# Performance work log

Measured on AMD Instinct MI355X. Metric: run time of the kernel, lower is better.

The kernel has to match this reference:

```python
import jax, jax.numpy as jnp
import numpy as np

H = 16
D_MODEL = 1024
D_K = D_MODEL // H


def setup_inputs() -> dict:
    key = jax.random.key(0)
    ks = jax.random.split(key, 12)
    B, S = 4, 2048
    scale = 1.0 / np.sqrt(D_MODEL)
    inp = {
        "query": jax.random.normal(ks[0], (B, S, D_MODEL), dtype=jnp.float32),
        "key": jax.random.normal(ks[1], (B, S, D_MODEL), dtype=jnp.float32),
        "value": jax.random.normal(ks[2], (B, S, D_MODEL), dtype=jnp.float32),
        "Wq": jax.random.normal(ks[3], (D_MODEL, D_MODEL), dtype=jnp.float32) * scale,
        "bq": jnp.zeros((D_MODEL,), dtype=jnp.float32),
        "Wk": jax.random.normal(ks[4], (D_MODEL, D_MODEL), dtype=jnp.float32) * scale,
        "bk": jnp.zeros((D_MODEL,), dtype=jnp.float32),
        "Wv": jax.random.normal(ks[5], (D_MODEL, D_MODEL), dtype=jnp.float32) * scale,
        "bv": jnp.zeros((D_MODEL,), dtype=jnp.float32),
        "Wo": jax.random.normal(ks[6], (D_MODEL, D_MODEL), dtype=jnp.float32) * scale,
        "bo": jnp.zeros((D_MODEL,), dtype=jnp.float32),
    }
    return inp


def reference(query, key, value, Wq, bq, Wk, bk, Wv, bv, Wo, bo):
    B, S, _ = query.shape
    # Linear projections (torch Linear: x @ W^T + b), then split heads -> [B,H,S,d_k]
    def proj(x, W, b):
        y = x @ W.T + b
        return y.reshape(B, S, H, D_K).transpose(0, 2, 1, 3)

    q = proj(query, Wq, bq)
    k = proj(key, Wk, bk)
    v = proj(value, Wv, bv)

    # Explicit QK^T / sqrt(d_k), softmax, AV (no mask; dropout = identity in eval)
    scores = jnp.einsum("bhqd,bhkd->bhqk", q, k) / jnp.sqrt(jnp.float32(D_K))
    attn = jax.nn.softmax(scores, axis=-1)
    x = jnp.einsum("bhqk,bhkd->bhqd", attn, v)

    # Merge heads and final output projection
    x = x.transpose(0, 2, 1, 3).reshape(B, S, H * D_K)
    return x @ Wo.T + bo
```

## Files before the change

kernel.cpp:

```cpp
#include <hip/hip_runtime.h>
#include <hip/hip_bf16.h>
#include <stdint.h>

#define BATCH 4
#define SEQ   2048
#define DM    1024
#define NH    16
#define DK    64
#define MROWS (BATCH * SEQ)

#define C1 0.1803368801111204f

typedef __attribute__((ext_vector_type(8))) short short8;
typedef __attribute__((ext_vector_type(4))) float f32x4;
typedef __attribute__((ext_vector_type(4))) float floatv4;
typedef __attribute__((ext_vector_type(4))) unsigned short us4;
typedef __attribute__((ext_vector_type(4))) unsigned int uint4v;

static __device__ __forceinline__ unsigned short f2bf(float f) {
    union { float f; uint32_t u; } c; c.f = f;
    uint32_t u = c.u;
    return (unsigned short)((u + 0x7fffu + ((u >> 16) & 1u)) >> 16);
}

static __device__ __forceinline__ unsigned int cvt_pk_bf16(float a, float b) {
    __hip_bfloat162 h = __float22bfloat162_rn(float2{a, b});
    unsigned int u; __builtin_memcpy(&u, &h, 4); return u;
}

#define AS1C(p) ((const __attribute__((address_space(1))) unsigned int*)(uintptr_t)(const void*)(p))
#define AS3(p)  ((__attribute__((address_space(3))) unsigned int*)(uintptr_t)(void*)(p))

__global__ __launch_bounds__(256) void cvt3_k(const float* __restrict__ a, const float* __restrict__ b,
                                              const float* __restrict__ c,
                                              unsigned short* __restrict__ oa, unsigned short* __restrict__ ob,
                                              unsigned short* __restrict__ oc) {
    const int z = blockIdx.y;
    const float* s = (z == 0) ? a : (z == 1) ? b : c;
    unsigned short* o = (z == 0) ? oa : (z == 1) ? ob : oc;
    int i = blockIdx.x * 256 + threadIdx.x;
    floatv4 v = ((const floatv4*)s)[i];
    us4 w; w.x = f2bf(v.x); w.y = f2bf(v.y); w.z = f2bf(v.z); w.w = f2bf(v.w);
    ((us4*)o)[i] = w;
}

__global__ __launch_bounds__(256) void cvt4_k(const float* __restrict__ a, const float* __restrict__ b,
                                              const float* __restrict__ c, const float* __restrict__ d,
                                              unsigned short* __restrict__ oa, unsigned short* __restrict__ ob,
                                              unsigned short* __restrict__ oc, unsigned short* __restrict__ od) {
    const int z = blockIdx.y;
    const float* s = (z == 0) ? a : (z == 1) ? b : (z == 2) ? c : d;
    unsigned short* o = (z == 0) ? oa : (z == 1) ? ob : (z == 2) ? oc : od;
    int i = blockIdx.x * 256 + threadIdx.x;
    floatv4 v = ((const floatv4*)s)[i];
    us4 w; w.x = f2bf(v.x); w.y = f2bf(v.y); w.z = f2bf(v.z); w.w = f2bf(v.w);
    ((us4*)o)[i] = w;
}

template <int MODE>
static __device__ __forceinline__ void gemm_body(const unsigned short* __restrict__ A,
                                                 const unsigned short* __restrict__ Bw,
                                                 const float* __restrict__ bias,
                                                 void* __restrict__ out, int m0, int n0,
                                                 float scale) {
    const int tid = threadIdx.x;
    const int wave = tid >> 6, lane = tid & 63, quad = lane >> 4, l16 = lane & 15;
    const int wr = wave & 1, wc = wave >> 1;

    __shared__ alignas(16) unsigned short As[128 * 32];
    __shared__ alignas(16) unsigned short Bs[128 * 32];

    f32x4 acc[4][4];
    #pragma unroll
    for (int i = 0; i < 4; i++)
        #pragma unroll
        for (int j = 0; j < 4; j++) acc[i][j] = (f32x4){0.f, 0.f, 0.f, 0.f};

    const int srow = lane >> 2;
    const int scol = (lane & 3) * 8;

    for (int k0 = 0; k0 < DM; k0 += 32) {
        __syncthreads();
        #pragma unroll
        for (int t = 0; t < 2; t++) {
            const int rr = wave * 32 + t * 16;
            __builtin_amdgcn_global_load_lds(AS1C(A  + (size_t)(m0 + rr + srow) * DM + k0 + scol),
                                             AS3(&As[rr * 32]), 16, 0, 0);
            __builtin_amdgcn_global_load_lds(AS1C(Bw + (size_t)(n0 + rr + srow) * DM + k0 + scol),
                                             AS3(&Bs[rr * 32]), 16, 0, 0);
        }
        __syncthreads();

        short8 af[4], bf[4];
        #pragma unroll
        for (int i = 0; i < 4; i++) af[i] = *(const short8*)&As[(wr * 64 + i * 16 + l16) * 32 + quad * 8];
        #pragma unroll
        for (int i = 0; i < 4; i++) bf[i] = *(const short8*)&Bs[(wc * 64 + i * 16 + l16) * 32 + quad * 8];
        #pragma unroll
        for (int i = 0; i < 4; i++)
            #pragma unroll
            for (int j = 0; j < 4; j++)
                acc[i][j] = __builtin_amdgcn_mfma_f32_16x16x32_bf16(af[i], bf[j], acc[i][j], 0, 0, 0);
    }

    #pragma unroll
    for (int j = 0; j < 4; j++) {
        const int n = n0 + wc * 64 + j * 16 + l16;
        const float bv = bias[n];
        #pragma unroll
        for (int i = 0; i < 4; i++) {
            #pragma unroll
            for (int r = 0; r < 4; r++) {
                const int mrow = m0 + wr * 64 + i * 16 + quad * 4 + r;
                float val = (acc[i][j][r] + bv) * scale;
                if (MODE == 0) {
                    int bb = mrow >> 11, ss = mrow & (SEQ - 1), hh = n >> 6, dd = n & (DK - 1);
                    ((unsigned short*)out)[((((size_t)bb * NH + hh) * SEQ + ss) << 6) + dd] = f2bf(val);
                } else {
                    ((float*)out)[(size_t)mrow * DM + n] = val;
                }
            }
        }
    }
}

__global__ __launch_bounds__(256, 2) void gemm_qkv_k(const unsigned short* qa, const unsigned short* ka,
                                                     const unsigned short* va, const unsigned short* wq,
                                                     const unsigned short* wk, const unsigned short* wv,
                                                     const float* bq, const float* bk, const float* bv,
                                                     unsigned short* qh, unsigned short* kh, unsigned short* vh) {
    const int z = blockIdx.z;
    const unsigned short* A = (z == 0) ? qa : (z == 1) ? ka : va;
    const unsigned short* W = (z == 0) ? wq : (z == 1) ? wk : wv;
    const float* bi = (z == 0) ? bq : (z == 1) ? bk : bv;
    unsigned short* o = (z == 0) ? qh : (z == 1) ? kh : vh;
    const float sc = (z == 0) ? C1 : 1.0f;
    gemm_body<0>(A, W, bi, o, blockIdx.x * 128, blockIdx.y * 128, sc);
}

__global__ __launch_bounds__(256, 2) void gemm_o_k(const unsigned short* xb, const unsigned short* wo,
                                                   const float* bo, float* out) {
    gemm_body<1>(xb, wo, bo, out, blockIdx.x * 128, blockIdx.y * 128, 1.0f);
}

__global__ __launch_bounds__(256) void vtrans_k(const unsigned short* __restrict__ Vh,
                                                unsigned short* __restrict__ Vt) {
    const int bh = blockIdx.y;
    const int t0 = blockIdx.x * 128;
    const unsigned short* src = Vh + (size_t)bh * SEQ * DK;
    unsigned short* dst = Vt + (size_t)bh * DK * SEQ;
    #pragma unroll
    for (int it = 0; it < 2; it++) {
        const int id = it * 256 + threadIdx.x;
        const int C8 = id & 15;
        const int dp = id >> 4;
        unsigned int v[8];
        #pragma unroll
        for (int j = 0; j < 8; j++) {
            const int key = ((C8 >> 2) << 5) + ((j >> 2) << 4) + ((C8 & 3) << 2) + (j & 3);
            v[j] = *(const unsigned int*)(src + (size_t)(t0 + key) * DK + dp * 2);
        }
        short8 r0, r1;
        #pragma unroll
        for (int j = 0; j < 8; j++) { r0[j] = (short)(v[j] & 0xffff); r1[j] = (short)(v[j] >> 16); }
        *(short8*)(dst + (size_t)(dp * 2    ) * SEQ + t0 + C8 * 8) = r0;
        *(short8*)(dst + (size_t)(dp * 2 + 1) * SEQ + t0 + C8 * 8) = r1;
    }
}

__global__ __launch_bounds__(256, 4) void flash_attn_k(const unsigned short* __restrict__ Qh,
                                                       const unsigned short* __restrict__ Kh,
                                                       const unsigned short* __restrict__ Vtc,
                                                       unsigned short* __restrict__ Xb) {
    const int tid = threadIdx.x;
    const int wave = tid >> 6, lane = tid & 63, quad = lane >> 4, l16 = lane & 15;
    const int h = blockIdx.y, b = blockIdx.z;
    const unsigned short* Qp = Qh  + (size_t)(b * NH + h) * SEQ * DK;
    const unsigned short* Kp = Kh  + (size_t)(b * NH + h) * SEQ * DK;
    const unsigned short* Vp = Vtc + (size_t)(b * NH + h) * DK * SEQ;
    const int q0 = blockIdx.x * 128 + wave * 32;

    __shared__ alignas(16) unsigned short kt[128][72];
    __shared__ alignas(16) unsigned short vt[64][136];

    short8 aq[2][2];
    #pragma unroll
    for (int m = 0; m < 2; m++)
        #pragma unroll
        for (int kk = 0; kk < 2; kk++)
            aq[m][kk] = *(const short8*)(Qp + (size_t)(q0 + m * 16 + l16) * DK + kk * 32 + quad * 8);

    short8 ones;
    #pragma unroll
    for (int j = 0; j < 8; j++) ones[j] = (short)0x3F80;

    f32x4 O[2][4];
    f32x4 lacc[2];
    #pragma unroll
    for (int m = 0; m < 2; m++) {
        #pragma unroll
        for (int db = 0; db < 4; db++) O[m][db] = (f32x4){0.f, 0.f, 0.f, 0.f};
        lacc[m] = (f32x4){0.f, 0.f, 0.f, 0.f};
    }

    for (int t0 = 0; t0 < SEQ; t0 += 128) {
        __syncthreads();
        #pragma unroll
        for (int it = 0; it < 4; it++) {
            const int id = it * 256 + tid;
            const int key = id >> 3, dg = (id & 7) * 8;
            *(short8*)&kt[key][dg] = *(const short8*)(Kp + (size_t)(t0 + key) * DK + dg);
        }
        #pragma unroll
        for (int it = 0; it < 4; it++) {
            const int id = it * 256 + tid;
            const int d = id >> 4, pc = (id & 15) * 8;
            *(short8*)&vt[d][pc] = *(const short8*)(Vp + (size_t)d * SEQ + t0 + pc);
        }
        __syncthreads();

        #pragma unroll
        for (int t = 0; t < 4; t++) {
            f32x4 s[2][2];
            #pragma unroll
            for (int m = 0; m < 2; m++)
                #pragma unroll
                for (int sb = 0; sb < 2; sb++) s[m][sb] = (f32x4){0.f, 0.f, 0.f, 0.f};

            #pragma unroll
            for (int kk = 0; kk < 2; kk++) {
                short8 bk0 = *(const short8*)&kt[(t * 2    ) * 16 + l16][kk * 32 + quad * 8];
                short8 bk1 = *(const short8*)&kt[(t * 2 + 1) * 16 + l16][kk * 32 + quad * 8];
                s[0][0] = __builtin_amdgcn_mfma_f32_16x16x32_bf16(bk0, aq[0][kk], s[0][0], 0, 0, 0);
                s[0][1] = __builtin_amdgcn_mfma_f32_16x16x32_bf16(bk1, aq[0][kk], s[0][1], 0, 0, 0);
                s[1][0] = __builtin_amdgcn_mfma_f32_16x16x32_bf16(bk0, aq[1][kk], s[1][0], 0, 0, 0);
                s[1][1] = __builtin_amdgcn_mfma_f32_16x16x32_bf16(bk1, aq[1][kk], s[1][1], 0, 0, 0);
            }

            short8 pa[2];
            #pragma unroll
            for (int m = 0; m < 2; m++) {
                uint4v pk;
                pk.x = cvt_pk_bf16(exp2f(s[m][0][0]), exp2f(s[m][0][1]));
                pk.y = cvt_pk_bf16(exp2f(s[m][0][2]), exp2f(s[m][0][3]));
                pk.z = cvt_pk_bf16(exp2f(s[m][1][0]), exp2f(s[m][1][1]));
                pk.w = cvt_pk_bf16(exp2f(s[m][1][2]), exp2f(s[m][1][3]));
                __builtin_memcpy(&pa[m], &pk, 16);
            }

            #pragma unroll
            for (int db = 0; db < 4; db++) {
                short8 vf = *(const short8*)&vt[db * 16 + l16][t * 32 + quad * 8];
                O[0][db] = __builtin_amdgcn_mfma_f32_16x16x32_bf16(pa[0], vf, O[0][db], 0, 0, 0);
                O[1][db] = __builtin_amdgcn_mfma_f32_16x16x32_bf16(pa[1], vf, O[1][db], 0, 0, 0);
            }
            lacc[0] = __builtin_amdgcn_mfma_f32_16x16x32_bf16(pa[0], ones, lacc[0], 0, 0, 0);
            lacc[1] = __builtin_amdgcn_mfma_f32_16x16x32_bf16(pa[1], ones, lacc[1], 0, 0, 0);
        }
    }

    #pragma unroll
    for (int m = 0; m < 2; m++) {
        #pragma unroll
        for (int r = 0; r < 4; r++) {
            const float inv = 1.f / lacc[m][r];
            const int srow = q0 + m * 16 + quad * 4 + r;
            unsigned short* op = Xb + ((size_t)b * SEQ + srow) * DM + h * DK;
            #pragma unroll
            for (int db = 0; db < 4; db++)
                op[db * 16 + l16] = f2bf(O[m][db][r] * inv);
        }
    }
}

extern "C" void kernel_launch(void* const* d_in, const int* in_sizes, int n_in,
                              void* d_out, int out_size, void* d_ws, size_t ws_size,
                              hipStream_t stream) {
    const float* q_in = (const float*)d_in[0];
    const float* k_in = (const float*)d_in[1];
    const float* v_in = (const float*)d_in[2];
    const float* Wq   = (const float*)d_in[3];
    const float* bq   = (const float*)d_in[4];
    const float* Wk   = (const float*)d_in[5];
    const float* bk   = (const float*)d_in[6];
    const float* Wv   = (const float*)d_in[7];
    const float* bv   = (const float*)d_in[8];
    const float* Wo   = (const float*)d_in[9];
    const float* bo   = (const float*)d_in[10];

    const size_t MB = 1024ull * 1024ull;
    char* ws = (char*)d_ws;
    unsigned short* qa  = (unsigned short*)(ws +   0 * MB);
    unsigned short* ka  = (unsigned short*)(ws +  16 * MB);
    unsigned short* va  = (unsigned short*)(ws +  32 * MB);
    unsigned short* wqb = (unsigned short*)(ws +  48 * MB);
    unsigned short* wkb = (unsigned short*)(ws +  50 * MB);
    unsigned short* wvb = (unsigned short*)(ws +  52 * MB);
    unsigned short* wob = (unsigned short*)(ws +  54 * MB);
    unsigned short* qh  = (unsigned short*)(ws +  56 * MB);
    unsigned short* kh  = (unsigned short*)(ws +  72 * MB);
    unsigned short* vh  = (unsigned short*)(ws +  88 * MB);
    unsigned short* xb  = (unsigned short*)(ws + 104 * MB);
    unsigned short* vtc = va;

    cvt3_k<<<dim3(8192, 3), 256, 0, stream>>>(q_in, k_in, v_in, qa, ka, va);
    cvt4_k<<<dim3(1024, 4), 256, 0, stream>>>(Wq, Wk, Wv, Wo, wqb, wkb, wvb, wob);

    gemm_qkv_k<<<dim3(MROWS / 128, DM / 128, 3), 256, 0, stream>>>(qa, ka, va, wqb, wkb, wvb,
                                                                   bq, bk, bv, qh, kh, vh);
    vtrans_k<<<dim3(SEQ / 128, BATCH * NH), 256, 0, stream>>>(vh, vtc);

    flash_attn_k<<<dim3(SEQ / 128, NH, BATCH), 256, 0, stream>>>(qh, kh, vtc, xb);

    gemm_o_k<<<dim3(MROWS / 128, DM / 128), 256, 0, stream>>>(xb, wob, bo, (float*)d_out);
}
```

Before: 387.0 us.

## Fuse V transpose into QKV GEMM epilogue and prefetch K/V tiles in attention

The V projection GEMM now writes its output directly in the transposed, permuted key order the attention kernel expects, so the separate transpose kernel and its extra read and write pass are gone. The flash attention loop now register-prefetches the next K and V tile while the current one is being computed, and it replaces the second __syncthreads with an LDS wait plus a raw barrier. exp2f is swapped for the hardware exp2 builtin. Risks include the key-permutation mapping in the epilogue and a small rise in register pressure from the prefetch buffers.

After: 338.3 us. -12.6%, faster.

```diff
diff --git a/kernel.cpp b/kernel.cpp
--- a/kernel.cpp
+++ b/kernel.cpp
@@ -27,6 +27,8 @@
     __hip_bfloat162 h = __float22bfloat162_rn(float2{a, b});
     unsigned int u; __builtin_memcpy(&u, &h, 4); return u;
 }
+
+static __device__ __forceinline__ float ex2(float x) { return __builtin_amdgcn_exp2f(x); }
 
 #define AS1C(p) ((const __attribute__((address_space(1))) unsigned int*)(uintptr_t)(const void*)(p))
 #define AS3(p)  ((__attribute__((address_space(3))) unsigned int*)(uintptr_t)(void*)(p))
@@ -109,15 +111,26 @@
         const float bv = bias[n];
         #pragma unroll
         for (int i = 0; i < 4; i++) {
-            #pragma unroll
-            for (int r = 0; r < 4; r++) {
-                const int mrow = m0 + wr * 64 + i * 16 + quad * 4 + r;
-                float val = (acc[i][j][r] + bv) * scale;
-                if (MODE == 0) {
-                    int bb = mrow >> 11, ss = mrow & (SEQ - 1), hh = n >> 6, dd = n & (DK - 1);
-                    ((unsigned short*)out)[((((size_t)bb * NH + hh) * SEQ + ss) << 6) + dd] = f2bf(val);
-                } else {
-                    ((float*)out)[(size_t)mrow * DM + n] = val;
+            if (MODE == 2) {
+                const int hh = n >> 6, dd = n & (DK - 1);
+                const int bb = m0 >> 11;
+                const size_t pos = (size_t)(m0 & (SEQ - 1))
+                                 + (size_t)((wr * 2 + (i >> 1)) * 32 + quad * 8 + (i & 1) * 4);
+                us4 w;
+                #pragma unroll
+                for (int r = 0; r < 4; r++) w[r] = f2bf(acc[i][j][r] + bv);
+                *(us4*)((unsigned short*)out + (((size_t)bb * NH + hh) * DK + dd) * SEQ + pos) = w;
+            } else {
+                #pragma unroll
+                for (int r = 0; r < 4; r++) {
+                    const int mrow = m0 + wr * 64 + i * 16 + quad * 4 + r;
+                    float val = (acc[i][j][r] + bv) * scale;
+                    if (MODE == 0) {
+                        int bb = mrow >> 11, ss = mrow & (SEQ - 1), hh = n >> 6, dd = n & (DK - 1);
+                        ((unsigned short*)out)[((((size_t)bb * NH + hh) * SEQ + ss) << 6) + dd] = f2bf(val);
+                    } else {
+                        ((float*)out)[(size_t)mrow * DM + n] = val;
+                    }
                 }
             }
         }
@@ -128,44 +141,23 @@
                                                      const unsigned short* va, const unsigned short* wq,
                                                      const unsigned short* wk, const unsigned short* wv,
                                                      const float* bq, const float* bk, const float* bv,
-                                                     unsigned short* qh, unsigned short* kh, unsigned short* vh) {
+                                                     unsigned short* qh, unsigned short* kh, unsigned short* vtc) {
     const int z = blockIdx.z;
-    const unsigned short* A = (z == 0) ? qa : (z == 1) ? ka : va;
-    const unsigned short* W = (z == 0) ? wq : (z == 1) ? wk : wv;
-    const float* bi = (z == 0) ? bq : (z == 1) ? bk : bv;
-    unsigned short* o = (z == 0) ? qh : (z == 1) ? kh : vh;
-    const float sc = (z == 0) ? C1 : 1.0f;
-    gemm_body<0>(A, W, bi, o, blockIdx.x * 128, blockIdx.y * 128, sc);
+    if (z == 2) {
+        gemm_body<2>(va, wv, bv, vtc, blockIdx.x * 128, blockIdx.y * 128, 1.0f);
+    } else {
+        const unsigned short* A = (z == 0) ? qa : ka;
+        const unsigned short* W = (z == 0) ? wq : wk;
+        const float* bi = (z == 0) ? bq : bk;
+        unsigned short* o = (z == 0) ? qh : kh;
+        const float sc = (z == 0) ? C1 : 1.0f;
+        gemm_body<0>(A, W, bi, o, blockIdx.x * 128, blockIdx.y * 128, sc);
+    }
 }
 
 __global__ __launch_bounds__(256, 2) void gemm_o_k(const unsigned short* xb, const unsigned short* wo,
                                                    const float* bo, float* out) {
     gemm_body<1>(xb, wo, bo, out, blockIdx.x * 128, blockIdx.y * 128, 1.0f);
-}
-
-__global__ __launch_bounds__(256) void vtrans_k(const unsigned short* __restrict__ Vh,
-                                                unsigned short* __restrict__ Vt) {
-    const int bh = blockIdx.y;
-    const int t0 = blockIdx.x * 128;
-    const unsigned short* src = Vh + (size_t)bh * SEQ * DK;
-    unsigned short* dst = Vt + (size_t)bh * DK * SEQ;
-    #pragma unroll
-    for (int it = 0; it < 2; it++) {
-        const int id = it * 256 + threadIdx.x;
-        const int C8 = id & 15;
-        const int dp = id >> 4;
-        unsigned int v[8];
-        #pragma unroll
-        for (int j = 0; j < 8; j++) {
-            const int key = ((C8 >> 2) << 5) + ((j >> 2) << 4) + ((C8 & 3) << 2) + (j & 3);
-            v[j] = *(const unsigned int*)(src + (size_t)(t0 + key) * DK + dp * 2);
-        }
-        short8 r0, r1;
-        #pragma unroll
-        for (int j = 0; j < 8; j++) { r0[j] = (short)(v[j] & 0xffff); r1[j] = (short)(v[j] >> 16); }
-        *(short8*)(dst + (size_t)(dp * 2    ) * SEQ + t0 + C8 * 8) = r0;
-        *(short8*)(dst + (size_t)(dp * 2 + 1) * SEQ + t0 + C8 * 8) = r1;
-    }
 }
 
 __global__ __launch_bounds__(256, 4) void flash_attn_k(const unsigned short* __restrict__ Qh,
@@ -203,21 +195,37 @@
         lacc[m] = (f32x4){0.f, 0.f, 0.f, 0.f};
     }
 
+    const unsigned short* kgp = Kp + (size_t)(tid >> 3) * DK + (tid & 7) * 8;
+    const unsigned short* vgp = Vp + (size_t)(tid >> 4) * SEQ + (tid & 15) * 8;
+    unsigned short* kws = &kt[tid >> 3][(tid & 7) * 8];
+    unsigned short* vws = &vt[tid >> 4][(tid & 15) * 8];
+
+    short8 krg[4], vrg[4];
+    #pragma unroll
+    for (int it = 0; it < 4; it++) {
+        krg[it] = *(const short8*)(kgp + (size_t)it * 32 * DK);
+        vrg[it] = *(const short8*)(vgp + (size_t)it * 16 * SEQ);
+    }
+    kgp += (size_t)128 * DK;
+    vgp += 128;
+
     for (int t0 = 0; t0 < SEQ; t0 += 128) {
         __syncthreads();
         #pragma unroll
         for (int it = 0; it < 4; it++) {
-            const int id = it * 256 + tid;
-            const int key = id >> 3, dg = (id & 7) * 8;
-            *(short8*)&kt[key][dg] = *(const short8*)(Kp + (size_t)(t0 + key) * DK + dg);
+            *(short8*)(kws + it * 32 * 72) = krg[it];
+            *(short8*)(vws + it * 16 * 136) = vrg[it];
         }
         #pragma unroll
         for (int it = 0; it < 4; it++) {
-            const int id = it * 256 + tid;
-            const int d = id >> 4, pc = (id & 15) * 8;
-            *(short8*)&vt[d][pc] = *(const short8*)(Vp + (size_t)d * SEQ + t0 + pc);
-        }
-        __syncthreads();
+            krg[it] = *(const short8*)(kgp + (size_t)it * 32 * DK);
+            vrg[it] = *(const short8*)(vgp + (size_t)it * 16 * SEQ);
+        }
+        kgp += (size_t)128 * DK;
+        vgp += 128;
+        asm volatile("s_waitcnt lgkmcnt(0)" ::: "memory");
+        __builtin_amdgcn_s_barrier();
+        __builtin_amdgcn_sched_barrier(0);
 
         #pragma unroll
         for (int t = 0; t < 4; t++) {
@@ -241,10 +249,10 @@
             #pragma unroll
             for (int m = 0; m < 2; m++) {
                 uint4v pk;
-                pk.x = cvt_pk_bf16(exp2f(s[m][0][0]), exp2f(s[m][0][1]));
-                pk.y = cvt_pk_bf16(exp2f(s[m][0][2]), exp2f(s[m][0][3]));
-                pk.z = cvt_pk_bf16(exp2f(s[m][1][0]), exp2f(s[m][1][1]));
-                pk.w = cvt_pk_bf16(exp2f(s[m][1][2]), exp2f(s[m][1][3]));
+                pk.x = cvt_pk_bf16(ex2(s[m][0][0]), ex2(s[m][0][1]));
+                pk.y = cvt_pk_bf16(ex2(s[m][0][2]), ex2(s[m][0][3]));
+                pk.z = cvt_pk_bf16(ex2(s[m][1][0]), ex2(s[m][1][1]));
+                pk.w = cvt_pk_bf16(ex2(s[m][1][2]), ex2(s[m][1][3]));
                 __builtin_memcpy(&pa[m], &pk, 16);
             }
 
@@ -299,16 +307,14 @@
     unsigned short* wob = (unsigned short*)(ws +  54 * MB);
     unsigned short* qh  = (unsigned short*)(ws +  56 * MB);
     unsigned short* kh  = (unsigned short*)(ws +  72 * MB);
-    unsigned short* vh  = (unsigned short*)(ws +  88 * MB);
+    unsigned short* vtc = (unsigned short*)(ws +  88 * MB);
     unsigned short* xb  = (unsigned short*)(ws + 104 * MB);
-    unsigned short* vtc = va;
 
     cvt3_k<<<dim3(8192, 3), 256, 0, stream>>>(q_in, k_in, v_in, qa, ka, va);
     cvt4_k<<<dim3(1024, 4), 256, 0, stream>>>(Wq, Wk, Wv, Wo, wqb, wkb, wvb, wob);
 
     gemm_qkv_k<<<dim3(MROWS / 128, DM / 128, 3), 256, 0, stream>>>(qa, ka, va, wqb, wkb, wvb,
-                                                                   bq, bk, bv, qh, kh, vh);
-    vtrans_k<<<dim3(SEQ / 128, BATCH * NH), 256, 0, stream>>>(vh, vtc);
+                                                                   bq, bk, bv, qh, kh, vtc);
 
     flash_attn_k<<<dim3(SEQ / 128, NH, BATCH), 256, 0, stream>>>(qh, kh, vtc, xb);
 
```
